# Performance work log

Hardware: AMD Instinct MI355X
Metric: run time of the kernel (lower is better)

Reference implementation:

```python
import jax, jax.numpy as jnp
import numpy as np

B, C, H, W = 16, 256, 80, 80
K = 3          # depthwise conv kernel size
ALPHA = 0.1    # EMA smoothing factor
EPS = 1e-7


def _decay(L):
    # computed in float64 then cast to float32, matching the torch buffer
    pos = np.arange(L, dtype=np.float64)
    return jnp.asarray(((1.0 - ALPHA) ** pos).astype(np.float32))


def setup_inputs() -> dict:
    key = jax.random.key(0)
    k1, k2, k3 = jax.random.split(key, 3)
    x = jax.random.normal(k1, (B, C, H, W), dtype=jnp.float32)
    bound = 1.0 / np.sqrt(K)  # torch Conv1d default init, fan_in = (in/groups)*K = K
    conv_w = jax.random.uniform(k2, (C, 1, K), minval=-bound, maxval=bound, dtype=jnp.float32)
    conv_b = jax.random.uniform(k3, (C,), minval=-bound, maxval=bound, dtype=jnp.float32)
    return {"x": x, "conv_w": conv_w, "conv_b": conv_b}


def reference(x, conv_w, conv_b):
    b, c, h, w = x.shape
    L = h * w
    decay = _decay(L)[None, None, :]          # [1,1,L]
    x_flat = x.reshape(b, c, L)               # [B,C,L]

    weighted = x_flat * (ALPHA * decay)
    cumsum = jnp.cumsum(weighted, axis=-1)
    cumsum_decay = jnp.cumsum(ALPHA * decay, axis=-1)   # [1,1,L]
    ema = cumsum / (cumsum_decay + EPS)

    conv = jax.lax.conv_general_dilated(
        x_flat, conv_w,
        window_strides=(1,),
        padding=[(K // 2, K // 2)],
        dimension_numbers=("NCH", "OIH", "NCH"),
        feature_group_count=c,
    ) + conv_b[None, :, None]

    out = (ema + conv).reshape(b, c, h, w)
    return out + x
```

## Files before the change

kernel.cpp:

```cpp
#include <hip/hip_runtime.h>
#include <math.h>

#define L_LEN 6400
#define NROWS 4096
#define C_CH 256
#define TPB 320
#define VPT 20
#define LOG2_DECAY_F -0.15200309f

typedef float v4f __attribute__((ext_vector_type(4)));

__device__ __forceinline__ void prefetch_row(const v4f* gsrc, v4f* ldst, int t) {
    const int wbase = t & ~63;
#pragma unroll
    for (int k = 0; k < 5; ++k) {
        __builtin_amdgcn_global_load_lds(
            (__attribute__((address_space(1))) void*)(gsrc + k * TPB + t),
            (__attribute__((address_space(3))) void*)(ldst + k * TPB + wbase),
            16, 0, 0);
    }
}

__global__ __launch_bounds__(TPB) void ema_attn_kernel(
    const float* __restrict__ x,
    const float* __restrict__ conv_w,
    const float* __restrict__ conv_b,
    float* __restrict__ out)
{
    __shared__ __align__(16) float sbuf[L_LEN];
    __shared__ float wsum[TPB / 64];

    const int row  = blockIdx.x;
    const int t    = threadIdx.x;
    const int lane = t & 63;
    const int wid  = t >> 6;
    const int start = t * VPT;
    const int c    = row & (C_CH - 1);

    prefetch_row((const v4f*)(x + (long)row * L_LEN), (v4f*)sbuf, t);

    const float w0   = conv_w[c * 3 + 0];
    const float w1   = conv_w[c * 3 + 1];
    const float w2   = conv_w[c * 3 + 2];
    const float bias = conv_b[c];

    const float d0 = exp2f((float)start * LOG2_DECAY_F);

    __syncthreads();

    float xv[VPT];
    const v4f* my4 = (const v4f*)(sbuf + start);
#pragma unroll
    for (int i = 0; i < 5; ++i) {
        v4f v = my4[i];
        xv[4*i+0] = v.x; xv[4*i+1] = v.y; xv[4*i+2] = v.z; xv[4*i+3] = v.w;
    }
    const float xl = (start == 0)           ? 0.f : sbuf[start - 1];
    const float xr = (start + VPT == L_LEN) ? 0.f : sbuf[start + VPT];

    float p = 0.f, w = 0.1f;
#pragma unroll
    for (int j = 0; j < VPT; ++j) { p = fmaf(xv[j], w, p); w *= 0.9f; }
    const float s = d0 * p;

    float inc = s;
#pragma unroll
    for (int off = 1; off < 64; off <<= 1) {
        float n = __shfl_up(inc, off, 64);
        if (lane >= off) inc += n;
    }
    if (lane == 63) wsum[wid] = inc;
    __syncthreads();

    float excl = inc - s;
#pragma unroll
    for (int wp = 0; wp < TPB / 64; ++wp)
        if (wp < wid) excl += wsum[wp];

    float o[VPT];
    float pj = 0.f; w = 0.1f;
#pragma unroll
    for (int j = 0; j < VPT; ++j) {
        pj = fmaf(xv[j], w, pj);
        float cum = fmaf(d0, pj, excl);
        float cd  = fmaf(-d0, 9.0f * w, 1.0f) + 1e-7f;
        float ema = cum * __builtin_amdgcn_rcpf(cd);
        float prev = (j == 0)       ? xl : xv[j-1];
        float nx   = (j == VPT-1)   ? xr : xv[j+1];
        float conv = fmaf(w0, prev, fmaf(w1, xv[j], fmaf(w2, nx, bias)));
        o[j] = ema + conv + xv[j];
        w *= 0.9f;
    }
    v4f* my4w = (v4f*)(sbuf + start);
#pragma unroll
    for (int i = 0; i < 5; ++i) {
        v4f ov = { o[4*i+0], o[4*i+1], o[4*i+2], o[4*i+3] };
        my4w[i] = ov;
    }
    __syncthreads();

    v4f* go = (v4f*)(out + (long)row * L_LEN);
    const v4f* c4 = (const v4f*)sbuf;
#pragma unroll
    for (int k = 0; k < 5; ++k)
        __builtin_nontemporal_store(c4[k * TPB + t], go + k * TPB + t);
}

extern "C" void kernel_launch(void* const* d_in, const int* in_sizes, int n_in,
                              void* d_out, int out_size, void* d_ws, size_t ws_size,
                              hipStream_t stream) {
    const float* x      = (const float*)d_in[0];
    const float* conv_w = (const float*)d_in[1];
    const float* conv_b = (const float*)d_in[2];
    float* out          = (float*)d_out;
    ema_attn_kernel<<<NROWS, TPB, 0, stream>>>(x, conv_w, conv_b, out);
}
```

Baseline: 36.40 us.

## Make row staging wave-local to drop block-wide barriers around load and store

Each wave now loads and later stores only the contiguous slice of the row that its own lanes process. The block-wide barriers before compute and before the store are replaced by per-wave s_waitcnt waits. The conv halo values at wave and row edges are read directly from global memory, so no lane depends on another wave's LDS data. This aims to cut barrier stalls and let waves progress independently. The cost is two extra scalar-ish global loads per thread and reliance on manual waitcnt correctness for LDS visibility.

```diff
diff --git a/kernel.cpp b/kernel.cpp
--- a/kernel.cpp
+++ b/kernel.cpp
@@ -6,20 +6,11 @@
 #define C_CH 256
 #define TPB 320
 #define VPT 20
+#define WPB (TPB / 64)
+#define F4W 320
 #define LOG2_DECAY_F -0.15200309f
 
 typedef float v4f __attribute__((ext_vector_type(4)));
-
-__device__ __forceinline__ void prefetch_row(const v4f* gsrc, v4f* ldst, int t) {
-    const int wbase = t & ~63;
-#pragma unroll
-    for (int k = 0; k < 5; ++k) {
-        __builtin_amdgcn_global_load_lds(
-            (__attribute__((address_space(1))) void*)(gsrc + k * TPB + t),
-            (__attribute__((address_space(3))) void*)(ldst + k * TPB + wbase),
-            16, 0, 0);
-    }
-}
 
 __global__ __launch_bounds__(TPB) void ema_attn_kernel(
     const float* __restrict__ x,
@@ -28,7 +19,7 @@
     float* __restrict__ out)
 {
     __shared__ __align__(16) float sbuf[L_LEN];
-    __shared__ float wsum[TPB / 64];
+    __shared__ float wsum[WPB];
 
     const int row  = blockIdx.x;
     const int t    = threadIdx.x;
@@ -37,7 +28,24 @@
     const int start = t * VPT;
     const int c    = row & (C_CH - 1);
 
-    prefetch_row((const v4f*)(x + (long)row * L_LEN), (v4f*)sbuf, t);
+    const long rowbase = (long)row * L_LEN;
+    const v4f* gsrc = (const v4f*)(x + rowbase);
+    v4f* lbase = (v4f*)sbuf;
+
+#pragma unroll
+    for (int k = 0; k < 5; ++k) {
+        __builtin_amdgcn_global_load_lds(
+            (__attribute__((address_space(1))) void*)(gsrc + wid * F4W + k * 64 + lane),
+            (__attribute__((address_space(3))) void*)(lbase + wid * F4W + k * 64),
+            16, 0, 0);
+    }
+
+    const int il = (start == 0) ? 0 : start - 1;
+    const int ir = (start + VPT >= L_LEN) ? (L_LEN - 1) : (start + VPT);
+    float gxl = x[rowbase + il];
+    float gxr = x[rowbase + ir];
+    if (start == 0) gxl = 0.f;
+    if (start + VPT >= L_LEN) gxr = 0.f;
 
     const float w0   = conv_w[c * 3 + 0];
     const float w1   = conv_w[c * 3 + 1];
@@ -46,7 +54,7 @@
 
     const float d0 = exp2f((float)start * LOG2_DECAY_F);
 
-    __syncthreads();
+    asm volatile("s_waitcnt vmcnt(0)" ::: "memory");
 
     float xv[VPT];
     const v4f* my4 = (const v4f*)(sbuf + start);
@@ -55,8 +63,6 @@
         v4f v = my4[i];
         xv[4*i+0] = v.x; xv[4*i+1] = v.y; xv[4*i+2] = v.z; xv[4*i+3] = v.w;
     }
-    const float xl = (start == 0)           ? 0.f : sbuf[start - 1];
-    const float xr = (start + VPT == L_LEN) ? 0.f : sbuf[start + VPT];
 
     float p = 0.f, w = 0.1f;
 #pragma unroll
@@ -74,7 +80,7 @@
 
     float excl = inc - s;
 #pragma unroll
-    for (int wp = 0; wp < TPB / 64; ++wp)
+    for (int wp = 0; wp < WPB; ++wp)
         if (wp < wid) excl += wsum[wp];
 
     float o[VPT];
@@ -85,8 +91,8 @@
         float cum = fmaf(d0, pj, excl);
         float cd  = fmaf(-d0, 9.0f * w, 1.0f) + 1e-7f;
         float ema = cum * __builtin_amdgcn_rcpf(cd);
-        float prev = (j == 0)       ? xl : xv[j-1];
-        float nx   = (j == VPT-1)   ? xr : xv[j+1];
+        float prev = (j == 0)       ? gxl : xv[j-1];
+        float nx   = (j == VPT-1)   ? gxr : xv[j+1];
         float conv = fmaf(w0, prev, fmaf(w1, xv[j], fmaf(w2, nx, bias)));
         o[j] = ema + conv + xv[j];
         w *= 0.9f;
@@ -97,13 +103,15 @@
         v4f ov = { o[4*i+0], o[4*i+1], o[4*i+2], o[4*i+3] };
         my4w[i] = ov;
     }
-    __syncthreads();
 
-    v4f* go = (v4f*)(out + (long)row * L_LEN);
-    const v4f* c4 = (const v4f*)sbuf;
+    asm volatile("s_waitcnt lgkmcnt(0)" ::: "memory");
+
+    v4f* go = (v4f*)(out + rowbase);
 #pragma unroll
-    for (int k = 0; k < 5; ++k)
-        __builtin_nontemporal_store(c4[k * TPB + t], go + k * TPB + t);
+    for (int k = 0; k < 5; ++k) {
+        const int i4 = wid * F4W + k * 64 + lane;
+        __builtin_nontemporal_store(lbase[i4], go + i4);
+    }
 }
 
 extern "C" void kernel_launch(void* const* d_in, const int* in_sizes, int n_in,
```

Result: no change. 36.19 us (-0.6%).
